# Performance work log

Hardware: AMD Instinct MI355X
Metric: run time of the kernel (lower is better)

The kernel has to match this reference:

```python
import jax, jax.numpy as jnp
import numpy as np

D = 200          # in_feat == out_feat
N = 20000        # num nodes
E = 320000       # num edges
R = 512          # num relation types


def setup_inputs() -> dict:
    key = jax.random.key(0)
    ks = jax.random.split(key, 12)
    # glorot-ish init scale for params
    def glorot(k, shape):
        fan = shape[0] + shape[1]
        return jax.random.normal(k, shape, dtype=jnp.float32) * jnp.sqrt(2.0 / fan)
    return {
        "node": jax.random.normal(ks[0], (N, D), dtype=jnp.float32),
        "rel": jax.random.normal(ks[1], (R, D), dtype=jnp.float32),
        "norm": jax.random.uniform(ks[2], (N, 1), dtype=jnp.float32),
        "fre": jax.random.uniform(ks[3], (E,), dtype=jnp.float32),
        "w_triplet": glorot(ks[4], (3 * D, D)),
        "w_quad": glorot(ks[5], (D, D)),
        "loop_weight": glorot(ks[6], (D, D)),
        "evolve_loop_weight": glorot(ks[7], (D, D)),
        "edge_src": jax.random.randint(ks[8], (E,), 0, N, dtype=jnp.int64).astype(jnp.int32),
        "edge_dst": jax.random.randint(ks[9], (E,), 0, N, dtype=jnp.int64).astype(jnp.int32),
        "edge_type": jax.random.randint(ks[10], (E,), 0, R, dtype=jnp.int64).astype(jnp.int32),
    }


def reference(node, rel, norm, fre, w_triplet, w_quad, loop_weight,
              evolve_loop_weight, edge_src, edge_dst, edge_type):
    n = node.shape[0]
    d = node.shape[1]
    # gather per-edge features
    src_h = node[edge_src]            # [E, D]
    dst_h = node[edge_dst]            # [E, D]
    rel_emb = rel[edge_type]          # [E, D]
    # quads_msg_func: concat([src,rel,dst]) @ w_triplet, split to avoid [E,3D] concat
    W_s, W_r, W_d = w_triplet[:d], w_triplet[d:2 * d], w_triplet[2 * d:]
    triplet = src_h @ W_s + rel_emb @ W_r + dst_h @ W_d   # [E, D]
    a = (triplet + fre[:, None]) @ w_quad                 # [E, D]
    a = jax.nn.leaky_relu(a, negative_slope=0.01)
    # edge softmax over incoming edges per destination node (per channel)
    seg_max = jax.ops.segment_max(a, edge_dst, num_segments=n)   # [N, D]
    ex = jnp.exp(a - seg_max[edge_dst])
    seg_sum = jax.ops.segment_sum(ex, edge_dst, num_segments=n)  # [N, D]
    att = ex / seg_sum[edge_dst]
    # weighted message aggregation + per-node norm
    h = jax.ops.segment_sum(att * triplet, edge_dst, num_segments=n)
    h = h * norm
    # self-loop: loop_weight where in_degree > 0, else evolve_loop_weight
    deg = jax.ops.segment_sum(jnp.ones((edge_dst.shape[0],), dtype=jnp.float32),
                              edge_dst, num_segments=n)
    loop_msg = jnp.where((deg > 0)[:, None],
                         node @ loop_weight,
                         node @ evolve_loop_weight)
    return jax.nn.relu(h + loop_msg)
```

## Files before the change

kernel.cpp:

```cpp
#include <hip/hip_runtime.h>
#include <hip/hip_bf16.h>
#include <cstdint>
#include <cstddef>

#define DD 200
#define NN 20000
#define EE 320000
#define RRR 512
#define KP 256
#define KREAL 224
#define MT 157
#define NT 10
#define RMT 4
#define RNT 4
#define NBLK_NODE (MT * NT)
#define NBLK_GEMM (NBLK_NODE + RMT * RNT)
#define NBLK_SCAT ((EE + 255) / 256)
#define LOG2E 1.4426950408889634f

#define PB_NODE 10000
#define PB_REL  (PB_NODE + 256)
#define PB_HIST (PB_REL + 1250)
#define PB_W    (PB_HIST + 200)
#define PB_CQ   (PB_W + 1)
#define PB_PAD  (PB_CQ + 196)

typedef __attribute__((ext_vector_type(8))) short bf16x8;
typedef __attribute__((ext_vector_type(4))) float f32x4;

__device__ __forceinline__ float bf2f_lo(unsigned int u) { return __uint_as_float(u << 16); }
__device__ __forceinline__ float bf2f_hi(unsigned int u) { return __uint_as_float(u & 0xffff0000u); }
__device__ __forceinline__ unsigned short f2bf(float f) {
  unsigned int x = __float_as_uint(f);
  return (unsigned short)((x + 0x7fffu + ((x >> 16) & 1u)) >> 16);
}
__device__ __forceinline__ unsigned int f2bf2(float a, float b) {
  return (unsigned int)f2bf(a) | ((unsigned int)f2bf(b) << 16);
}
__device__ __forceinline__ void gl_lds16(const unsigned short* g, unsigned short* l) {
  __builtin_amdgcn_global_load_lds(
      (const __attribute__((address_space(1))) void*)g,
      (__attribute__((address_space(3))) void*)l, 16, 0, 0);
}

__global__ __launch_bounds__(256) void kPrep(const float* __restrict__ node, const float* __restrict__ rel,
                                             const int* __restrict__ dst,
                                             const float* __restrict__ wt, const float* __restrict__ wq,
                                             const float* __restrict__ lw, const float* __restrict__ elw,
                                             unsigned int* __restrict__ Au, unsigned int* __restrict__ Arelu,
                                             int* __restrict__ deg,
                                             unsigned short* __restrict__ Bt, unsigned short* __restrict__ BtRel,
                                             float* __restrict__ cq) {
  int b = blockIdx.x, t = threadIdx.x;
  if (b < PB_NODE) {
    int h = t >> 7, tt = t & 127;
    int n = b * 2 + h;
    unsigned v = 0;
    if (tt < 100) { float2 f = ((const float2*)(node + (size_t)n * DD))[tt]; v = f2bf2(f.x, f.y); }
    Au[(size_t)n * 128 + tt] = v;
  } else if (b < PB_REL) {
    int h = t >> 7, tt = t & 127;
    int r = (b - PB_NODE) * 2 + h;
    unsigned v = 0;
    if (tt < 100) { float2 f = ((const float2*)(rel + (size_t)r * DD))[tt]; v = f2bf2(f.x, f.y); }
    Arelu[(size_t)r * 128 + tt] = v;
  } else if (b < PB_HIST) {
    int e = (b - PB_REL) * 256 + t;
    if (e < EE) atomicAdd(&deg[dst[e]], 1);
  } else if (b < PB_W) {
    int k = b - PB_HIST, j = t;
    if (j >= DD) return;
    const float* w0 = wt + (size_t)k * DD;
    const float* w1 = wt + (size_t)(2 * DD + k) * DD;
    const float* w2 = wt + (size_t)(DD + k) * DD;
    float s0 = 0.f, s1 = 0.f, s2 = 0.f;
    for (int i = 0; i < DD; ++i) {
      float q = wq[i * DD + j];
      s0 = fmaf(w0[i], q, s0);
      s1 = fmaf(w1[i], q, s1);
      s2 = fmaf(w2[i], q, s2);
    }
    Bt[(2 * j) * KP + k]       = f2bf(w0[j]);
    Bt[(2 * j + 1) * KP + k]   = f2bf(s0 * LOG2E);
    Bt[(400 + 2 * j) * KP + k] = f2bf(w1[j]);
    Bt[(401 + 2 * j) * KP + k] = f2bf(s1 * LOG2E);
    Bt[(800 + 2 * j) * KP + k] = f2bf(lw[k * DD + j]);
    Bt[(801 + 2 * j) * KP + k] = f2bf(elw[k * DD + j]);
    BtRel[(2 * j) * KP + k]     = f2bf(w2[j]);
    BtRel[(2 * j + 1) * KP + k] = f2bf(s2 * LOG2E);
  } else if (b < PB_CQ) {
    int j = t; if (j >= DD) return;
    float s = 0.f;
    for (int i = 0; i < DD; ++i) s += wq[i * DD + j];
    cq[j] = s * LOG2E;
  } else {
    int idx = (b - PB_CQ) * 256 + t;
    ((unsigned int*)Bt)[(idx / 28) * 128 + 100 + idx % 28] = 0;
  }
}

__global__ __launch_bounds__(1024) void k_scan(const int* __restrict__ deg, int* __restrict__ offs) {
  __shared__ int wsum[16];
  int tid = threadIdx.x, lane = tid & 63, wv = tid >> 6;
  const int4* deg4 = (const int4*)deg;
  int4* offs4 = (int4*)offs;
  int4 v[5]; int ps[5]; int tsum = 0;
#pragma unroll
  for (int c = 0; c < 5; ++c) {
    int idx = tid * 5 + c;
    v[c] = (idx < 5000) ? deg4[idx] : make_int4(0, 0, 0, 0);
    ps[c] = tsum;
    tsum += v[c].x + v[c].y + v[c].z + v[c].w;
  }
  int x = tsum;
#pragma unroll
  for (int off = 1; off < 64; off <<= 1) {
    int y = __shfl_up(x, off, 64);
    if (lane >= off) x += y;
  }
  if (lane == 63) wsum[wv] = x;
  __syncthreads();
  if (wv == 0) {
    int w = (lane < 16) ? wsum[lane] : 0;
#pragma unroll
    for (int off = 1; off < 16; off <<= 1) {
      int y = __shfl_up(w, off, 64);
      if (lane >= off) w += y;
    }
    if (lane < 16) wsum[lane] = w;
  }
  __syncthreads();
  int pre = ((wv > 0) ? wsum[wv - 1] : 0) + x - tsum;
#pragma unroll
  for (int c = 0; c < 5; ++c) {
    int idx = tid * 5 + c;
    if (idx < 5000) {
      int a = pre + ps[c];
      int bq = a + v[c].x, cc = bq + v[c].y, d = cc + v[c].z;
      offs4[idx] = make_int4(a, bq, cc, d);
    }
  }
  if (tid == 0) offs[NN] = wsum[15];
}

__global__ __launch_bounds__(256) void k_gs(const unsigned short* __restrict__ A,
                                            const unsigned short* __restrict__ Bt,
                                            unsigned short* __restrict__ NT2u,
                                            const unsigned short* __restrict__ Arel,
                                            const unsigned short* __restrict__ BtRel,
                                            unsigned short* __restrict__ RelPu,
                                            const int* __restrict__ esrc, const int* __restrict__ edst,
                                            const int* __restrict__ etyp, const float* __restrict__ fre,
                                            const int* __restrict__ offs, int* __restrict__ cursor,
                                            int2* __restrict__ erec) {
  __shared__ unsigned short As[128 * 32];
  __shared__ unsigned short Bs[128 * 32];
  if (blockIdx.x >= NBLK_GEMM) {
    int e = (blockIdx.x - NBLK_GEMM) * 256 + threadIdx.x;
    if (e >= EE) return;
    int d = edst[e];
    int p = offs[d] + atomicAdd(&cursor[d], 1);
    erec[p] = make_int2(esrc[e] | (etyp[e] << 15), __float_as_int(fre[e]));
    return;
  }
  bool isrel = blockIdx.x >= NBLK_NODE;
  int bid, ntn;
  const unsigned short *Ag, *Bg;
  if (!isrel) { bid = blockIdx.x; ntn = NT; Ag = A; Bg = Bt; }
  else        { bid = blockIdx.x - NBLK_NODE; ntn = RNT; Ag = Arel; Bg = BtRel; }
  int mt = bid / ntn, nt = bid % ntn;
  int t = threadIdx.x, lane = t & 63, wv = t >> 6;
  int lr = lane & 15, k8 = lane >> 4;
  int wm = (wv >> 1) * 64, wn = (wv & 1) * 64;
  int sr = wv * 16 + (lane >> 2);
  int sc = lane & 3;
  f32x4 acc[4][4] = {};
  Ag += (size_t)(mt * 128) * KP;
  Bg += (size_t)(nt * 128) * KP;
  for (int kk = 0; kk < KREAL; kk += 32) {
#pragma unroll
    for (int i = 0; i < 2; ++i) {
      int row = i * 64 + sr;
      int gcol = kk + ((sc ^ (row & 3)) << 3);
      gl_lds16(Ag + (size_t)row * KP + gcol, As + i * 2048 + wv * 512);
      gl_lds16(Bg + (size_t)row * KP + gcol, Bs + i * 2048 + wv * 512);
    }
    __syncthreads();
    bf16x8 af[4], bfr[4];
#pragma unroll
    for (int mi = 0; mi < 4; ++mi) {
      int row = wm + mi * 16 + lr;
      af[mi] = *(const bf16x8*)(As + row * 32 + ((k8 ^ (row & 3)) << 3));
      int col = wn + mi * 16 + lr;
      bfr[mi] = *(const bf16x8*)(Bs + col * 32 + ((k8 ^ (col & 3)) << 3));
    }
#pragma unroll
    for (int mi = 0; mi < 4; ++mi)
#pragma unroll
      for (int ni = 0; ni < 4; ++ni)
        acc[mi][ni] = __builtin_amdgcn_mfma_f32_16x16x32_bf16(af[mi], bfr[ni], acc[mi][ni], 0, 0, 0);
    __syncthreads();
  }
  int rb = k8 * 4;
#pragma unroll
  for (int mi = 0; mi < 4; ++mi)
#pragma unroll
    for (int ni = 0; ni < 4; ++ni) {
      int col = nt * 128 + wn + ni * 16 + lr;
      if (!isrel) {
        if (col < 1200) {
          int g = col / 400, w = col - g * 400;
          unsigned short* dst = NT2u + (size_t)g * NN * 400 + w;
#pragma unroll
          for (int r = 0; r < 4; ++r) {
            int row = mt * 128 + wm + mi * 16 + rb + r;
            if (row < NN) dst[(size_t)row * 400] = f2bf(acc[mi][ni][r]);
          }
        }
      } else {
        if (col < 400) {
#pragma unroll
          for (int r = 0; r < 4; ++r) {
            int row = mt * 128 + wm + mi * 16 + rb + r;
            RelPu[(size_t)row * 400 + col] = f2bf(acc[mi][ni][r]);
          }
        }
      }
    }
}

__global__ __launch_bounds__(128) void k_agg(const uint2* __restrict__ GS2,
                                             const uint2* __restrict__ GD2,
                                             const uint2* __restrict__ GL2,
                                             const uint2* __restrict__ Rel2,
                                             const float2* __restrict__ cq2,
                                             const float* __restrict__ norm,
                                             const int* __restrict__ offs,
                                             const int2* __restrict__ erec,
                                             float* __restrict__ out) {
  int n = blockIdx.x;
  int j2 = threadIdx.x;
  if (j2 >= 100) return;
  int e0 = offs[n], e1 = offs[n + 1];
  uint2 dp = GD2[(size_t)n * 100 + j2];
  float xd0 = bf2f_lo(dp.x), xq0 = bf2f_hi(dp.x);
  float xd1 = bf2f_lo(dp.y), xq1 = bf2f_hi(dp.y);
  float2 cqv = cq2[j2];
  float s0 = 0.f, s1 = 0.f, num0 = 0.f, num1 = 0.f;
#define DO_EDGE(SP, RP, FI)                                                   \
  {                                                                           \
    float F = __int_as_float(FI);                                             \
    float t0 = bf2f_lo(SP.x) + bf2f_lo(RP.x);                                 \
    float a0 = bf2f_hi(SP.x) + bf2f_hi(RP.x) + fmaf(F, cqv.x, xq0);           \
    float t1 = bf2f_lo(SP.y) + bf2f_lo(RP.y);                                 \
    float a1 = bf2f_hi(SP.y) + bf2f_hi(RP.y) + fmaf(F, cqv.y, xq1);           \
    a0 = fmaxf(a0, 0.01f * a0); a1 = fmaxf(a1, 0.01f * a1);                   \
    float ev0 = exp2f(a0), ev1 = exp2f(a1);                                   \
    s0 += ev0; num0 = fmaf(ev0, t0, num0);                                    \
    s1 += ev1; num1 = fmaf(ev1, t1, num1);                                    \
  }
#define LOADB(R, GS, GR, base)                                                \
  {                                                                           \
    _Pragma("unroll")                                                         \
    for (int u = 0; u < 4; ++u) R[u] = erec[(base) + u];                      \
    _Pragma("unroll")                                                         \
    for (int u = 0; u < 4; ++u) GS[u] = GS2[((unsigned)R[u].x & 0x7fffu) * 100u + j2]; \
    _Pragma("unroll")                                                         \
    for (int u = 0; u < 4; ++u) GR[u] = Rel2[((unsigned)R[u].x >> 15) * 100u + j2];    \
  }
#define COMPB(R, GS, GR)                                                      \
  {                                                                           \
    _Pragma("unroll")                                                         \
    for (int u = 0; u < 4; ++u) DO_EDGE(GS[u], GR[u], R[u].y)                 \
  }
  int cnt = e1 - e0;
  int nb = cnt >> 2;
  int2 rA[4], rB[4];
  uint2 gsA[4], grA[4], gsB[4], grB[4];
  if (nb > 0) LOADB(rA, gsA, grA, e0)
  int b = 1;
  for (; b + 1 < nb; b += 2) {
    LOADB(rB, gsB, grB, e0 + b * 4)
    COMPB(rA, gsA, grA)
    LOADB(rA, gsA, grA, e0 + (b + 1) * 4)
    COMPB(rB, gsB, grB)
  }
  if (b < nb) {
    LOADB(rB, gsB, grB, e0 + b * 4)
    COMPB(rA, gsA, grA)
    COMPB(rB, gsB, grB)
  } else if (nb > 0) {
    COMPB(rA, gsA, grA)
  }
  for (int i = e0 + nb * 4; i < e1; ++i) {
    int2 r = erec[i];
    uint2 g = GS2[((unsigned)r.x & 0x7fffu) * 100u + j2];
    uint2 R = Rel2[((unsigned)r.x >> 15) * 100u + j2];
    DO_EDGE(g, R, r.y)
  }
#undef COMPB
#undef LOADB
#undef DO_EDGE
  uint2 lp = GL2[(size_t)n * 100 + j2];
  float o0, o1;
  if (e1 > e0) {
    float nm = norm[n];
    o0 = (num0 / s0 + xd0) * nm + bf2f_lo(lp.x);
    o1 = (num1 / s1 + xd1) * nm + bf2f_lo(lp.y);
  } else {
    o0 = bf2f_hi(lp.x);
    o1 = bf2f_hi(lp.y);
  }
  ((float2*)(out + (size_t)n * DD))[j2] = make_float2(fmaxf(o0, 0.f), fmaxf(o1, 0.f));
}

extern "C" void kernel_launch(void* const* d_in, const int* in_sizes, int n_in,
                              void* d_out, int out_size, void* d_ws, size_t ws_size,
                              hipStream_t stream) {
  const float* node = (const float*)d_in[0];
  const float* rel  = (const float*)d_in[1];
  const float* norm = (const float*)d_in[2];
  const float* fre  = (const float*)d_in[3];
  const float* wt   = (const float*)d_in[4];
  const float* wq   = (const float*)d_in[5];
  const float* lw   = (const float*)d_in[6];
  const float* elw  = (const float*)d_in[7];
  const int* esrc = (const int*)d_in[8];
  const int* edst = (const int*)d_in[9];
  const int* etyp = (const int*)d_in[10];
  float* out = (float*)d_out;

  char* p = (char*)d_ws;
  auto carve = [&](size_t bytes) -> char* {
    char* r = p; p += (bytes + 255) & ~(size_t)255; return r;
  };
  unsigned short* A     = (unsigned short*)carve((size_t)(MT * 128) * KP * 2);
  unsigned short* Arel  = (unsigned short*)carve((size_t)RRR * KP * 2);
  unsigned short* BtAll = (unsigned short*)carve((size_t)(1280 + 512) * KP * 2);
  unsigned short* NT2   = (unsigned short*)carve((size_t)3 * NN * 400 * 2);
  unsigned short* RelP  = (unsigned short*)carve((size_t)RRR * 400 * 2);
  float* cq   = (float*)carve((size_t)DD * 4);
  int* degcur = (int*)carve((size_t)2 * NN * 4);
  int* offs   = (int*)carve((size_t)(NN + 1) * 4);
  int2* erec  = (int2*)carve((size_t)EE * 8);

  unsigned short* Bt    = BtAll;
  unsigned short* BtRel = BtAll + (size_t)1280 * KP;
  int* deg    = degcur;
  int* cursor = degcur + NN;

  const uint2* GS2 = (const uint2*)NT2;
  const uint2* GD2 = GS2 + (size_t)NN * 100;
  const uint2* GL2 = GS2 + (size_t)2 * NN * 100;

  hipMemsetAsync(degcur, 0, (size_t)2 * NN * 4, stream);
  kPrep<<<PB_PAD, 256, 0, stream>>>(node, rel, edst, wt, wq, lw, elw,
                                    (unsigned int*)A, (unsigned int*)Arel, deg, Bt, BtRel, cq);
  k_scan<<<1, 1024, 0, stream>>>(deg, offs);
  k_gs<<<NBLK_GEMM + NBLK_SCAT, 256, 0, stream>>>(A, Bt, NT2, Arel, BtRel, RelP,
                                                  esrc, edst, etyp, fre, offs, cursor, erec);
  k_agg<<<NN, 128, 0, stream>>>(GS2, GD2, GL2, (const uint2*)RelP, (const float2*)cq,
                                norm, offs, erec, out);
}
```

Before: 134.2 us.

## Stage GEMM epilogue through LDS and widen aggregation gathers to uint4

The GEMM epilogue now writes bf16 results into shared memory in two phases and then emits coalesced 32-bit stores per row, replacing the scattered 16-bit strided stores. The aggregation kernel maps one wavefront per node, with 50 lanes each handling 4 channels through 16-byte gathers and 4 nodes per block. This is meant to cut the number of memory transactions on both the store side and the gather side. In exchange, the software double-buffered prefetch is dropped, 14 of every 64 lanes sit idle, and two extra syncs are added to the epilogue.

```diff
diff --git a/kernel.cpp b/kernel.cpp
--- a/kernel.cpp
+++ b/kernel.cpp
@@ -145,16 +145,15 @@
 
 __global__ __launch_bounds__(256) void k_gs(const unsigned short* __restrict__ A,
                                             const unsigned short* __restrict__ Bt,
-                                            unsigned short* __restrict__ NT2u,
+                                            unsigned int* __restrict__ NT2u32,
                                             const unsigned short* __restrict__ Arel,
                                             const unsigned short* __restrict__ BtRel,
-                                            unsigned short* __restrict__ RelPu,
+                                            unsigned int* __restrict__ RelPu32,
                                             const int* __restrict__ esrc, const int* __restrict__ edst,
                                             const int* __restrict__ etyp, const float* __restrict__ fre,
                                             const int* __restrict__ offs, int* __restrict__ cursor,
                                             int2* __restrict__ erec) {
-  __shared__ unsigned short As[128 * 32];
-  __shared__ unsigned short Bs[128 * 32];
+  __shared__ unsigned short SM[8192];
   if (blockIdx.x >= NBLK_GEMM) {
     int e = (blockIdx.x - NBLK_GEMM) * 256 + threadIdx.x;
     if (e >= EE) return;
@@ -163,6 +162,8 @@
     erec[p] = make_int2(esrc[e] | (etyp[e] << 15), __float_as_int(fre[e]));
     return;
   }
+  unsigned short* As = SM;
+  unsigned short* Bs = SM + 4096;
   bool isrel = blockIdx.x >= NBLK_NODE;
   int bid, ntn;
   const unsigned short *Ag, *Bg;
@@ -202,116 +203,116 @@
     __syncthreads();
   }
   int rb = k8 * 4;
-#pragma unroll
-  for (int mi = 0; mi < 4; ++mi)
-#pragma unroll
-    for (int ni = 0; ni < 4; ++ni) {
-      int col = nt * 128 + wn + ni * 16 + lr;
-      if (!isrel) {
-        if (col < 1200) {
-          int g = col / 400, w = col - g * 400;
-          unsigned short* dst = NT2u + (size_t)g * NN * 400 + w;
-#pragma unroll
-          for (int r = 0; r < 4; ++r) {
-            int row = mt * 128 + wm + mi * 16 + rb + r;
-            if (row < NN) dst[(size_t)row * 400] = f2bf(acc[mi][ni][r]);
-          }
-        }
-      } else {
-        if (col < 400) {
-#pragma unroll
-          for (int r = 0; r < 4; ++r) {
-            int row = mt * 128 + wm + mi * 16 + rb + r;
-            RelPu[(size_t)row * 400 + col] = f2bf(acc[mi][ni][r]);
-          }
+  const unsigned int* SMu = (const unsigned int*)SM;
+#pragma unroll
+  for (int ph = 0; ph < 2; ++ph) {
+    if ((wv & 1) == ph) {
+#pragma unroll
+      for (int mi = 0; mi < 4; ++mi)
+#pragma unroll
+        for (int ni = 0; ni < 4; ++ni)
+#pragma unroll
+          for (int r = 0; r < 4; ++r)
+            SM[(wm + mi * 16 + rb + r) * 64 + ni * 16 + lr] = f2bf(acc[mi][ni][r]);
+    }
+    __syncthreads();
+    int c = t & 31;
+    int colg = nt * 128 + ph * 64 + c * 2;
+    if (!isrel) {
+      if (colg < 1200) {
+        int g = colg / 400, w = colg - g * 400;
+        unsigned int* dstp = NT2u32 + (size_t)g * NN * 200 + (w >> 1);
+        for (int rr = t >> 5; rr < 128; rr += 8) {
+          int row = mt * 128 + rr;
+          if (row < NN) dstp[(size_t)row * 200] = SMu[rr * 32 + c];
         }
       }
-    }
-}
-
-__global__ __launch_bounds__(128) void k_agg(const uint2* __restrict__ GS2,
-                                             const uint2* __restrict__ GD2,
-                                             const uint2* __restrict__ GL2,
-                                             const uint2* __restrict__ Rel2,
-                                             const float2* __restrict__ cq2,
+    } else {
+      if (colg < 400) {
+        unsigned int* dstp = RelPu32 + (colg >> 1);
+        for (int rr = t >> 5; rr < 128; rr += 8) {
+          int row = mt * 128 + rr;
+          dstp[(size_t)row * 200] = SMu[rr * 32 + c];
+        }
+      }
+    }
+    __syncthreads();
+  }
+}
+
+__global__ __launch_bounds__(256) void k_agg(const uint4* __restrict__ GS4,
+                                             const uint4* __restrict__ GD4,
+                                             const uint4* __restrict__ GL4,
+                                             const uint4* __restrict__ Rel4,
+                                             const float4* __restrict__ cq4,
                                              const float* __restrict__ norm,
                                              const int* __restrict__ offs,
                                              const int2* __restrict__ erec,
                                              float* __restrict__ out) {
-  int n = blockIdx.x;
-  int j2 = threadIdx.x;
-  if (j2 >= 100) return;
+  int wv = threadIdx.x >> 6, lane = threadIdx.x & 63;
+  int n = blockIdx.x * 4 + wv;
+  if (lane >= 50) return;
   int e0 = offs[n], e1 = offs[n + 1];
-  uint2 dp = GD2[(size_t)n * 100 + j2];
-  float xd0 = bf2f_lo(dp.x), xq0 = bf2f_hi(dp.x);
-  float xd1 = bf2f_lo(dp.y), xq1 = bf2f_hi(dp.y);
-  float2 cqv = cq2[j2];
-  float s0 = 0.f, s1 = 0.f, num0 = 0.f, num1 = 0.f;
-#define DO_EDGE(SP, RP, FI)                                                   \
+  uint4 dp = GD4[(size_t)n * 50 + lane];
+  float xq0 = bf2f_hi(dp.x), xq1 = bf2f_hi(dp.y), xq2 = bf2f_hi(dp.z), xq3 = bf2f_hi(dp.w);
+  float4 cqv = cq4[lane];
+  float s0 = 0.f, s1 = 0.f, s2 = 0.f, s3 = 0.f;
+  float num0 = 0.f, num1 = 0.f, num2 = 0.f, num3 = 0.f;
+  const uint4* GSl = GS4 + lane;
+  const uint4* Rll = Rel4 + lane;
+#define DO_CH(GU, RU, XQ, CQ, S, NUM)                                         \
+  {                                                                           \
+    float tt = bf2f_lo(GU) + bf2f_lo(RU);                                     \
+    float aa = bf2f_hi(GU) + bf2f_hi(RU) + fmaf(F, CQ, XQ);                   \
+    aa = fmaxf(aa, 0.01f * aa);                                               \
+    float ev = exp2f(aa);                                                     \
+    S += ev; NUM = fmaf(ev, tt, NUM);                                         \
+  }
+#define DO_EDGE(G, R, FI)                                                     \
   {                                                                           \
     float F = __int_as_float(FI);                                             \
-    float t0 = bf2f_lo(SP.x) + bf2f_lo(RP.x);                                 \
-    float a0 = bf2f_hi(SP.x) + bf2f_hi(RP.x) + fmaf(F, cqv.x, xq0);           \
-    float t1 = bf2f_lo(SP.y) + bf2f_lo(RP.y);                                 \
-    float a1 = bf2f_hi(SP.y) + bf2f_hi(RP.y) + fmaf(F, cqv.y, xq1);           \
-    a0 = fmaxf(a0, 0.01f * a0); a1 = fmaxf(a1, 0.01f * a1);                   \
-    float ev0 = exp2f(a0), ev1 = exp2f(a1);                                   \
-    s0 += ev0; num0 = fmaf(ev0, t0, num0);                                    \
-    s1 += ev1; num1 = fmaf(ev1, t1, num1);                                    \
-  }
-#define LOADB(R, GS, GR, base)                                                \
-  {                                                                           \
-    _Pragma("unroll")                                                         \
-    for (int u = 0; u < 4; ++u) R[u] = erec[(base) + u];                      \
-    _Pragma("unroll")                                                         \
-    for (int u = 0; u < 4; ++u) GS[u] = GS2[((unsigned)R[u].x & 0x7fffu) * 100u + j2]; \
-    _Pragma("unroll")                                                         \
-    for (int u = 0; u < 4; ++u) GR[u] = Rel2[((unsigned)R[u].x >> 15) * 100u + j2];    \
-  }
-#define COMPB(R, GS, GR)                                                      \
-  {                                                                           \
-    _Pragma("unroll")                                                         \
-    for (int u = 0; u < 4; ++u) DO_EDGE(GS[u], GR[u], R[u].y)                 \
-  }
-  int cnt = e1 - e0;
-  int nb = cnt >> 2;
-  int2 rA[4], rB[4];
-  uint2 gsA[4], grA[4], gsB[4], grB[4];
-  if (nb > 0) LOADB(rA, gsA, grA, e0)
-  int b = 1;
-  for (; b + 1 < nb; b += 2) {
-    LOADB(rB, gsB, grB, e0 + b * 4)
-    COMPB(rA, gsA, grA)
-    LOADB(rA, gsA, grA, e0 + (b + 1) * 4)
-    COMPB(rB, gsB, grB)
-  }
-  if (b < nb) {
-    LOADB(rB, gsB, grB, e0 + b * 4)
-    COMPB(rA, gsA, grA)
-    COMPB(rB, gsB, grB)
-  } else if (nb > 0) {
-    COMPB(rA, gsA, grA)
-  }
-  for (int i = e0 + nb * 4; i < e1; ++i) {
+    DO_CH(G.x, R.x, xq0, cqv.x, s0, num0)                                     \
+    DO_CH(G.y, R.y, xq1, cqv.y, s1, num1)                                     \
+    DO_CH(G.z, R.z, xq2, cqv.z, s2, num2)                                     \
+    DO_CH(G.w, R.w, xq3, cqv.w, s3, num3)                                     \
+  }
+  int i = e0;
+  for (; i + 4 <= e1; i += 4) {
+    int2 r0 = erec[i], r1 = erec[i + 1], r2 = erec[i + 2], r3 = erec[i + 3];
+    uint4 g0 = GSl[(unsigned)(r0.x & 0x7fff) * 50u];
+    uint4 g1 = GSl[(unsigned)(r1.x & 0x7fff) * 50u];
+    uint4 g2 = GSl[(unsigned)(r2.x & 0x7fff) * 50u];
+    uint4 g3 = GSl[(unsigned)(r3.x & 0x7fff) * 50u];
+    uint4 R0 = Rll[((unsigned)r0.x >> 15) * 50u];
+    uint4 R1 = Rll[((unsigned)r1.x >> 15) * 50u];
+    uint4 R2 = Rll[((unsigned)r2.x >> 15) * 50u];
+    uint4 R3 = Rll[((unsigned)r3.x >> 15) * 50u];
+    DO_EDGE(g0, R0, r0.y)
+    DO_EDGE(g1, R1, r1.y)
+    DO_EDGE(g2, R2, r2.y)
+    DO_EDGE(g3, R3, r3.y)
+  }
+  for (; i < e1; ++i) {
     int2 r = erec[i];
-    uint2 g = GS2[((unsigned)r.x & 0x7fffu) * 100u + j2];
-    uint2 R = Rel2[((unsigned)r.x >> 15) * 100u + j2];
+    uint4 g = GSl[(unsigned)(r.x & 0x7fff) * 50u];
+    uint4 R = Rll[((unsigned)r.x >> 15) * 50u];
     DO_EDGE(g, R, r.y)
   }
-#undef COMPB
-#undef LOADB
 #undef DO_EDGE
-  uint2 lp = GL2[(size_t)n * 100 + j2];
-  float o0, o1;
+#undef DO_CH
+  uint4 lp = GL4[(size_t)n * 50 + lane];
+  float4 o;
   if (e1 > e0) {
     float nm = norm[n];
-    o0 = (num0 / s0 + xd0) * nm + bf2f_lo(lp.x);
-    o1 = (num1 / s1 + xd1) * nm + bf2f_lo(lp.y);
+    o.x = (num0 / s0 + bf2f_lo(dp.x)) * nm + bf2f_lo(lp.x);
+    o.y = (num1 / s1 + bf2f_lo(dp.y)) * nm + bf2f_lo(lp.y);
+    o.z = (num2 / s2 + bf2f_lo(dp.z)) * nm + bf2f_lo(lp.z);
+    o.w = (num3 / s3 + bf2f_lo(dp.w)) * nm + bf2f_lo(lp.w);
   } else {
-    o0 = bf2f_hi(lp.x);
-    o1 = bf2f_hi(lp.y);
-  }
-  ((float2*)(out + (size_t)n * DD))[j2] = make_float2(fmaxf(o0, 0.f), fmaxf(o1, 0.f));
+    o.x = bf2f_hi(lp.x); o.y = bf2f_hi(lp.y); o.z = bf2f_hi(lp.z); o.w = bf2f_hi(lp.w);
+  }
+  o.x = fmaxf(o.x, 0.f); o.y = fmaxf(o.y, 0.f); o.z = fmaxf(o.z, 0.f); o.w = fmaxf(o.w, 0.f);
+  ((float4*)(out + (size_t)n * DD))[lane] = o;
 }
 
 extern "C" void kernel_launch(void* const* d_in, const int* in_sizes, int n_in,
@@ -349,16 +350,17 @@
   int* deg    = degcur;
   int* cursor = degcur + NN;
 
-  const uint2* GS2 = (const uint2*)NT2;
-  const uint2* GD2 = GS2 + (size_t)NN * 100;
-  const uint2* GL2 = GS2 + (size_t)2 * NN * 100;
+  const uint4* GS4 = (const uint4*)NT2;
+  const uint4* GD4 = GS4 + (size_t)NN * 50;
+  const uint4* GL4 = GS4 + (size_t)2 * NN * 50;
 
   hipMemsetAsync(degcur, 0, (size_t)2 * NN * 4, stream);
   kPrep<<<PB_PAD, 256, 0, stream>>>(node, rel, edst, wt, wq, lw, elw,
                                     (unsigned int*)A, (unsigned int*)Arel, deg, Bt, BtRel, cq);
   k_scan<<<1, 1024, 0, stream>>>(deg, offs);
-  k_gs<<<NBLK_GEMM + NBLK_SCAT, 256, 0, stream>>>(A, Bt, NT2, Arel, BtRel, RelP,
+  k_gs<<<NBLK_GEMM + NBLK_SCAT, 256, 0, stream>>>(A, Bt, (unsigned int*)NT2, Arel, BtRel,
+                                                  (unsigned int*)RelP,
                                                   esrc, edst, etyp, fre, offs, cursor, erec);
-  k_agg<<<NN, 128, 0, stream>>>(GS2, GD2, GL2, (const uint2*)RelP, (const float2*)cq,
-                                norm, offs, erec, out);
-}
+  k_agg<<<NN / 4, 256, 0, stream>>>(GS4, GD4, GL4, (const uint4*)RelP, (const float4*)cq,
+                                    norm, offs, erec, out);
+}
```

Measured after the change: 147.3 us. 1.1x slower.
